# Kernel tuning notes

Measured on AMD Instinct MI355X. Metric: run time of the kernel, lower is better.

The kernel has to match this reference:

```python
import jax, jax.numpy as jnp
import numpy as np

MIN_SPARSITY = 0.05
MAX_SPARSITY = 0.3


def setup_inputs() -> dict:
    key = jax.random.key(0)
    k1, k2, k3 = jax.random.split(key, 3)
    B, D = 4096, 4096
    H = D // 4
    x = jax.random.normal(k1, (B, D), dtype=jnp.float32)
    W1 = jax.random.normal(k2, (D, H), dtype=jnp.float32) * (1.0 / np.sqrt(D))
    b1 = jnp.zeros((H,), dtype=jnp.float32)
    W2 = jax.random.normal(k3, (H, 1), dtype=jnp.float32) * (1.0 / np.sqrt(H))
    b2 = jnp.zeros((1,), dtype=jnp.float32)
    return {"x": x, "W1": W1, "b1": b1, "W2": W2, "b2": b2}


def reference(x, W1, b1, W2, b2):
    B, D = x.shape
    # learned per-row sparsity in [min, max]
    h = jax.nn.relu(x @ W1 + b1)                      # [B, D//4]
    s = jax.nn.sigmoid(h @ W2 + b2)                   # [B, 1]
    sparsity = MIN_SPARSITY + (MAX_SPARSITY - MIN_SPARSITY) * s  # [B, 1]

    # per-row kth smallest |x| as threshold; k = max(1, round(D*(1-sparsity)))
    abs_x = jnp.abs(x)
    sorted_abs = jnp.sort(abs_x, axis=1)              # [B, D] ascending
    k = jnp.round(D * (1.0 - sparsity[:, 0])).astype(jnp.int32)
    k = jnp.clip(k, 1, D)
    threshold = jnp.take_along_axis(sorted_abs, (k - 1)[:, None], axis=1)  # [B, 1]

    mask = (abs_x > threshold).astype(x.dtype)        # [B, D]
    sparse_x = x * mask
    actual_sparsity = mask.sum(axis=1) / D            # [B]
    l1_reg = jnp.abs(sparse_x).sum(axis=1).mean()     # scalar
    return sparse_x, mask, sparsity, actual_sparsity, l1_reg
```

## Files before the change

### kernel.cpp

```cpp
#include <hip/hip_runtime.h>
#include <hip/hip_fp8.h>

typedef __attribute__((ext_vector_type(4))) float f32x4;


__device__ __forceinline__ unsigned char f2fp8(float f) {
    return (unsigned char)__hip_cvt_float_to_fp8(f, __HIP_SATFINITE, __HIP_E4M3);
}

__device__ __forceinline__ void gl16(const void* g, void* l) {
    __builtin_amdgcn_global_load_lds(
        (const __attribute__((address_space(1))) void*)g,
        (__attribute__((address_space(3))) void*)l, 16, 0, 0);
}

__global__ __launch_bounds__(256) void k0a_cvtx(const float* __restrict__ x,
                                                unsigned char* __restrict__ xa_t)
{
    const int bm = blockIdx.x;
    const int ktbase = blockIdx.y * 16;
    const int t = threadIdx.x;
    const int rr = t >> 2, q = t & 3;
    const int kgp = q ^ ((rr >> 1) & 3);
    const size_t rowoff = (size_t)(bm * 64 + rr) * 4096;

    #pragma unroll
    for (int i = 0; i < 16; i++) {
        const int kt = ktbase + i;
        const float* src = x + rowoff + kt * 32 + q * 8;
        float4 v0 = *(const float4*)src;
        float4 v1 = *(const float4*)(src + 4);
        union { unsigned char c[8]; uint2 u; } o;
        o.c[0] = f2fp8(v0.x); o.c[1] = f2fp8(v0.y);
        o.c[2] = f2fp8(v0.z); o.c[3] = f2fp8(v0.w);
        o.c[4] = f2fp8(v1.x); o.c[5] = f2fp8(v1.y);
        o.c[6] = f2fp8(v1.z); o.c[7] = f2fp8(v1.w);
        *(uint2*)(xa_t + ((size_t)(bm * 128 + kt) * 64 + rr) * 32 + kgp * 8) = o.u;
    }
}

__global__ __launch_bounds__(256) void k0b_cvtw(const float* __restrict__ W1,
                                                unsigned char* __restrict__ wb_t)
{
    __shared__ float ls[32][128];
    const int bx = blockIdx.x;
    const int bn = bx >> 7, kt = bx & 127;
    const int t = threadIdx.x;

    #pragma unroll
    for (int i = 0; i < 4; i++) {
        int s = t + i * 256;
        int r = s >> 5, c4 = s & 31;
        *(float4*)&ls[r][c4 * 4] =
            *(const float4*)(W1 + (size_t)(kt * 32 + r) * 1024 + bn * 128 + c4 * 4);
    }
    __syncthreads();

    const int n = t >> 1, half = t & 1;
    #pragma unroll
    for (int kg2 = 0; kg2 < 2; kg2++) {
        const int kg = half * 2 + kg2;
        const int kgp = kg ^ ((n >> 1) & 3);
        union { unsigned char c[8]; uint2 u; } o;
        #pragma unroll
        for (int j = 0; j < 8; j++) o.c[j] = f2fp8(ls[kg * 8 + j][n] * 64.0f);
        *(uint2*)(wb_t + (size_t)(bn * 128 + kt) * 4096 + n * 32 + kgp * 8) = o.u;
    }
}

__global__ __launch_bounds__(512, 4) void k1est(const unsigned char* __restrict__ xa_t,
                                                const unsigned char* __restrict__ wb_t,
                                                const float* __restrict__ b1,
                                                const float* __restrict__ W2,
                                                float* __restrict__ plogit)
{
    __shared__ alignas(16) unsigned char Ab[4][4096];
    __shared__ alignas(16) unsigned char Bb[4][8192];

    const int bid = blockIdx.x;
    const int wgid = (bid & 7) * 64 + (bid >> 3);
    const int bn = wgid >> 6, bm = wgid & 63;
    const int tid = threadIdx.x;
    const int l = tid & 63, w = tid >> 6;
    const int wm = w & 3, wn = w >> 2;
    const int arow = l & 15, kg = l >> 4;
    const int kgs = kg ^ ((arow >> 1) & 3);
    const bool stager = (w < 4);

    const unsigned char* abase = xa_t + (size_t)bm * 128 * 2048;
    const unsigned char* bbase = wb_t + (size_t)bn * 128 * 4096;

    f32x4 acc[4];
    #pragma unroll
    for (int j = 0; j < 4; j++) acc[j] = (f32x4)0.0f;

#define ISSUE(step, buf)                                                          \
    if (stager) {                                                                 \
        gl16(abase + (size_t)(step) * 4096 + tid * 16, &Ab[buf][tid * 16]);       \
        gl16(bbase + (size_t)(step) * 8192 + tid * 16, &Bb[buf][tid * 16]);       \
        gl16(bbase + (size_t)(step) * 8192 + (256 + tid) * 16,                    \
             &Bb[buf][(256 + tid) * 16]);                                         \
    }

    ISSUE(0, 0);
    ISSUE(1, 1);

    for (int t = 0; t < 64; t++) {
        const int buf = t & 3;
        if (t <= 61) {
            ISSUE(t + 2, (t + 2) & 3);
            asm volatile("s_waitcnt vmcnt(6)" ::: "memory");
        } else if (t == 62) {
            asm volatile("s_waitcnt vmcnt(3)" ::: "memory");
        } else {
            asm volatile("s_waitcnt vmcnt(0)" ::: "memory");
        }
        __builtin_amdgcn_s_barrier();
        __builtin_amdgcn_sched_barrier(0);

        #pragma unroll
        for (int j = 0; j < 2; j++) {
            long af = *(const long*)&Ab[buf][j * 2048 + (wm * 16 + arow) * 32 + kgs * 8];
            #pragma unroll
            for (int nf = 0; nf < 4; nf++) {
                long bf = *(const long*)&Bb[buf][j * 4096 +
                                                 (wn * 64 + nf * 16 + arow) * 32 + kgs * 8];
                acc[nf] = __builtin_amdgcn_mfma_f32_16x16x32_fp8_fp8(af, bf, acc[nf], 0, 0, 0);
            }
        }
    }
#undef ISSUE

    float p[4] = {0.0f, 0.0f, 0.0f, 0.0f};
    #pragma unroll
    for (int nf = 0; nf < 4; nf++) {
        const int n = bn * 128 + wn * 64 + nf * 16 + arow;
        const float bb = b1[n], ww = W2[n];
        #pragma unroll
        for (int i = 0; i < 4; i++) {
            float h = acc[nf][i] * 0.015625f + bb;
            if (h > 0.0f) p[i] += h * ww;
        }
    }
    #pragma unroll
    for (int i = 0; i < 4; i++) {
        #pragma unroll
        for (int o = 1; o < 16; o <<= 1) p[i] += __shfl_xor(p[i], o, 64);
        if (arow == 0) {
            const int row = bm * 64 + wm * 16 + kg * 4 + i;
            plogit[(size_t)row * 16 + bn * 2 + wn] = p[i];
        }
    }
}

__global__ __launch_bounds__(256) void k2_row(const float* __restrict__ x,
                                              const float* __restrict__ plogit,
                                              const float* __restrict__ b2,
                                              float* __restrict__ out_sparse,
                                              float* __restrict__ out_mask,
                                              float* __restrict__ out_spars,
                                              float* __restrict__ out_actual,
                                              double* __restrict__ l1rows)
{
    __shared__ unsigned hist[2048];
    __shared__ unsigned cand[512];
    __shared__ unsigned wsum[4];
    __shared__ int cnt_w[4];
    __shared__ double l1_w[4];
    __shared__ unsigned sel_s, selexc_s;
    __shared__ int k_s;

    const int row = blockIdx.x;
    const int tid = threadIdx.x;
    const int lane = tid & 63, wid = tid >> 6;
    const float* xr = x + (size_t)row * 4096;

    for (int i = tid; i < 2048; i += 256) hist[i] = 0;
    if (tid == 0) {
        float lg = 0.0f;
        #pragma unroll
        for (int t = 0; t < 16; t++) lg += plogit[(size_t)row * 16 + t];
        double s  = 1.0 / (1.0 + exp(-(double)(lg + b2[0])));
        double sp = 0.05 + 0.25 * s;
        int k = (int)rint(4096.0 * (1.0 - sp));
        if (k < 1) k = 1;
        if (k > 4096) k = 4096;
        k_s = k;
        out_spars[row] = (float)sp;
    }
    __syncthreads();

    uint4 rv[4];
    #pragma unroll
    for (int j = 0; j < 4; j++) {
        rv[j] = ((const uint4*)xr)[tid + j * 256];
        atomicAdd(&hist[(rv[j].x & 0x7fffffffu) >> 20], 1u);
        atomicAdd(&hist[(rv[j].y & 0x7fffffffu) >> 20], 1u);
        atomicAdd(&hist[(rv[j].z & 0x7fffffffu) >> 20], 1u);
        atomicAdd(&hist[(rv[j].w & 0x7fffffffu) >> 20], 1u);
    }
    __syncthreads();

    int krem = k_s;
    unsigned prefix = 0;
    {
        const unsigned base = tid * 8;
        unsigned bl[8];
        unsigned v = 0;
        #pragma unroll
        for (int j = 0; j < 8; j++) { bl[j] = hist[base + j]; v += bl[j]; }
        unsigned sc = v;
        #pragma unroll
        for (int o = 1; o < 64; o <<= 1) {
            unsigned n = __shfl_up(sc, o, 64);
            if (lane >= o) sc += n;
        }
        if (lane == 63) wsum[wid] = sc;
        __syncthreads();
        unsigned off = 0;
        for (int ww = 0; ww < wid; ww++) off += wsum[ww];
        sc += off;
        unsigned exc = sc - v;
        if ((int)sc >= krem && (int)exc < krem) {
            unsigned run = exc;
            #pragma unroll
            for (int j = 0; j < 8; j++) {
                if ((int)run < krem && (int)(run + bl[j]) >= krem) {
                    sel_s = base + j; selexc_s = run;
                }
                run += bl[j];
            }
        }
        __syncthreads();
        prefix = sel_s;
        krem -= (int)selexc_s;
        __syncthreads();
    }

    int cntm = 0;
    #pragma unroll
    for (int j = 0; j < 4; j++)
        #pragma unroll
        for (int e = 0; e < 4; e++) {
            unsigned a = (&rv[j].x)[e] & 0x7fffffffu;
            if ((a >> 20) == prefix) cntm++;
        }
    unsigned sc2 = (unsigned)cntm;
    #pragma unroll
    for (int o = 1; o < 64; o <<= 1) {
        unsigned n = __shfl_up(sc2, o, 64);
        if (lane >= o) sc2 += n;
    }
    if (lane == 63) wsum[wid] = sc2;
    __syncthreads();
    unsigned off2 = 0;
    for (int ww = 0; ww < wid; ww++) off2 += wsum[ww];
    unsigned pos = sc2 + off2 - (unsigned)cntm;
    const int nc = (int)(wsum[0] + wsum[1] + wsum[2] + wsum[3]);
    #pragma unroll
    for (int j = 0; j < 4; j++)
        #pragma unroll
        for (int e = 0; e < 4; e++) {
            unsigned a = (&rv[j].x)[e] & 0x7fffffffu;
            if ((a >> 20) == prefix) { if (pos < 512) cand[pos] = a; pos++; }
        }
    __syncthreads();
    const bool usec = (nc <= 512);

    #pragma unroll
    for (int p = 0; p < 3; p++) {
        const int shift = (p == 0) ? 12 : (p == 1) ? 4 : 0;
        const int width = (p == 2) ? 4 : 8;
        const int nb = 1 << width;
        const int topshift = shift + width;
        if (tid < nb) hist[tid] = 0;
        __syncthreads();
        if (usec) {
            for (int i = tid; i < nc; i += 256) {
                unsigned a = cand[i];
                if ((a >> topshift) == prefix)
                    atomicAdd(&hist[(a >> shift) & (nb - 1)], 1u);
            }
        } else {
            #pragma unroll
            for (int j = 0; j < 4; j++) {
                #pragma unroll
                for (int e = 0; e < 4; e++) {
                    unsigned a = (&rv[j].x)[e] & 0x7fffffffu;
                    if ((a >> topshift) == prefix)
                        atomicAdd(&hist[(a >> shift) & (nb - 1)], 1u);
                }
            }
        }
        __syncthreads();
        unsigned v = (tid < nb) ? hist[tid] : 0;
        unsigned sc = v;
        #pragma unroll
        for (int o = 1; o < 64; o <<= 1) {
            unsigned n = __shfl_up(sc, o, 64);
            if (lane >= o) sc += n;
        }
        if (lane == 63) wsum[wid] = sc;
        __syncthreads();
        unsigned off = 0;
        for (int ww = 0; ww < wid; ww++) off += wsum[ww];
        sc += off;
        unsigned exc = sc - v;
        if ((int)sc >= krem && (int)exc < krem) { sel_s = (unsigned)tid; selexc_s = exc; }
        __syncthreads();
        prefix = (prefix << width) | sel_s;
        krem -= (int)selexc_s;
        __syncthreads();
    }
    const unsigned thr = prefix;

    int cnt = 0;
    double l1 = 0.0;
    float* os = out_sparse + (size_t)row * 4096;
    float* om = out_mask + (size_t)row * 4096;
    #pragma unroll
    for (int j = 0; j < 4; j++) {
        float4 sv, mv;
        #pragma unroll
        for (int e = 0; e < 4; e++) {
            unsigned b = (&rv[j].x)[e];
            unsigned a = b & 0x7fffffffu;
            bool m = a > thr;
            (&sv.x)[e] = m ? __uint_as_float(b) : 0.0f;
            (&mv.x)[e] = m ? 1.0f : 0.0f;
            if (m) { cnt++; l1 += (double)__uint_as_float(a); }
        }
        ((float4*)os)[tid + j * 256] = sv;
        ((float4*)om)[tid + j * 256] = mv;
    }
    #pragma unroll
    for (int o = 32; o > 0; o >>= 1) {
        cnt += __shfl_down(cnt, o, 64);
        l1  += __shfl_down(l1,  o, 64);
    }
    if (lane == 0) { cnt_w[wid] = cnt; l1_w[wid] = l1; }
    __syncthreads();
    if (tid == 0) {
        int c    = cnt_w[0] + cnt_w[1] + cnt_w[2] + cnt_w[3];
        double l = l1_w[0] + l1_w[1] + l1_w[2] + l1_w[3];
        out_actual[row] = (float)c / 4096.0f;
        l1rows[row] = l;
    }
}

__global__ __launch_bounds__(1024) void k3_l1(const double* __restrict__ l1rows,
                                              float* __restrict__ out_l1)
{
    __shared__ double sm[1024];
    int tid = threadIdx.x;
    double s = l1rows[tid] + l1rows[tid + 1024] + l1rows[tid + 2048] + l1rows[tid + 3072];
    sm[tid] = s;
    __syncthreads();
    for (int st = 512; st > 0; st >>= 1) {
        if (tid < st) sm[tid] += sm[tid + st];
        __syncthreads();
    }
    if (tid == 0) out_l1[0] = (float)(sm[0] / 4096.0);
}

extern "C" void kernel_launch(void* const* d_in, const int* in_sizes, int n_in,
                              void* d_out, int out_size, void* d_ws, size_t ws_size,
                              hipStream_t stream)
{
    const float* x  = (const float*)d_in[0];
    const float* W1 = (const float*)d_in[1];
    const float* b1 = (const float*)d_in[2];
    const float* W2 = (const float*)d_in[3];
    const float* b2 = (const float*)d_in[4];

    float* out        = (float*)d_out;
    float* out_sparse = out;
    float* out_mask   = out + 16777216;
    float* out_spars  = out + 33554432;
    float* out_actual = out + 33558528;
    float* out_l1     = out + 33562624;

    unsigned char* xa_t = (unsigned char*)(out);
    unsigned char* wb_t = (unsigned char*)(out + 4194304);

    char* ws = (char*)d_ws;
    float*  plogit = (float*)(ws);
    double* l1rows = (double*)(ws + 262144);

    k0a_cvtx<<<dim3(64, 8), 256, 0, stream>>>(x, xa_t);
    k0b_cvtw<<<1024, 256, 0, stream>>>(W1, wb_t);
    k1est<<<512, 512, 0, stream>>>(xa_t, wb_t, b1, W2, plogit);
    k2_row<<<4096, 256, 0, stream>>>(x, plogit, b2, out_sparse, out_mask,
                                     out_spars, out_actual, l1rows);
    k3_l1<<<1, 1024, 0, stream>>>(l1rows, out_l1);
}
```

Baseline: 109.7 us.

## Split row selection and mask application into separate kernels with nontemporal stores

Splits the per-row threshold-selection kernel into two: one finds the per-row threshold and stores it to workspace, and a second re-reads x and writes the sparse and mask outputs with nontemporal stores. The aim is to shorten the selection kernel and let the write-heavy phase run at full occupancy with streaming stores. In exchange, x is read from global memory a second time and there is an extra kernel launch.

```diff
diff --git a/kernel.cpp b/kernel.cpp
--- a/kernel.cpp
+++ b/kernel.cpp
@@ -2,6 +2,7 @@
 #include <hip/hip_fp8.h>
 
 typedef __attribute__((ext_vector_type(4))) float f32x4;
+typedef __attribute__((ext_vector_type(4))) unsigned u32x4;
 
 
 __device__ __forceinline__ unsigned char f2fp8(float f) {
@@ -153,20 +154,15 @@
     }
 }
 
-__global__ __launch_bounds__(256) void k2_row(const float* __restrict__ x,
-                                              const float* __restrict__ plogit,
-                                              const float* __restrict__ b2,
-                                              float* __restrict__ out_sparse,
-                                              float* __restrict__ out_mask,
-                                              float* __restrict__ out_spars,
-                                              float* __restrict__ out_actual,
-                                              double* __restrict__ l1rows)
+__global__ __launch_bounds__(256) void k2a_sel(const float* __restrict__ x,
+                                               const float* __restrict__ plogit,
+                                               const float* __restrict__ b2,
+                                               unsigned* __restrict__ thr_arr,
+                                               float* __restrict__ out_spars)
 {
     __shared__ unsigned hist[2048];
     __shared__ unsigned cand[512];
     __shared__ unsigned wsum[4];
-    __shared__ int cnt_w[4];
-    __shared__ double l1_w[4];
     __shared__ unsigned sel_s, selexc_s;
     __shared__ int k_s;
 
@@ -312,26 +308,45 @@
         krem -= (int)selexc_s;
         __syncthreads();
     }
-    const unsigned thr = prefix;
+
+    if (tid == 0) thr_arr[row] = prefix;
+}
+
+__global__ __launch_bounds__(256) void k2b_apply(const float* __restrict__ x,
+                                                 const unsigned* __restrict__ thr_arr,
+                                                 float* __restrict__ out_sparse,
+                                                 float* __restrict__ out_mask,
+                                                 float* __restrict__ out_actual,
+                                                 double* __restrict__ l1rows)
+{
+    __shared__ int cnt_w[4];
+    __shared__ double l1_w[4];
+
+    const int row = blockIdx.x;
+    const int tid = threadIdx.x;
+    const int lane = tid & 63, wid = tid >> 6;
+    const unsigned thr = thr_arr[row];
+    const float* xr = x + (size_t)row * 4096;
+    f32x4* os = (f32x4*)(out_sparse + (size_t)row * 4096);
+    f32x4* om = (f32x4*)(out_mask + (size_t)row * 4096);
 
     int cnt = 0;
     double l1 = 0.0;
-    float* os = out_sparse + (size_t)row * 4096;
-    float* om = out_mask + (size_t)row * 4096;
     #pragma unroll
     for (int j = 0; j < 4; j++) {
-        float4 sv, mv;
+        u32x4 bv = ((const u32x4*)xr)[tid + j * 256];
+        f32x4 sv, mv;
         #pragma unroll
         for (int e = 0; e < 4; e++) {
-            unsigned b = (&rv[j].x)[e];
+            unsigned b = bv[e];
             unsigned a = b & 0x7fffffffu;
             bool m = a > thr;
-            (&sv.x)[e] = m ? __uint_as_float(b) : 0.0f;
-            (&mv.x)[e] = m ? 1.0f : 0.0f;
+            sv[e] = m ? __uint_as_float(b) : 0.0f;
+            mv[e] = m ? 1.0f : 0.0f;
             if (m) { cnt++; l1 += (double)__uint_as_float(a); }
         }
-        ((float4*)os)[tid + j * 256] = sv;
-        ((float4*)om)[tid + j * 256] = mv;
+        __builtin_nontemporal_store(sv, &os[tid + j * 256]);
+        __builtin_nontemporal_store(mv, &om[tid + j * 256]);
     }
     #pragma unroll
     for (int o = 32; o > 0; o >>= 1) {
@@ -384,13 +399,15 @@
     unsigned char* wb_t = (unsigned char*)(out + 4194304);
 
     char* ws = (char*)d_ws;
-    float*  plogit = (float*)(ws);
-    double* l1rows = (double*)(ws + 262144);
+    float*    plogit  = (float*)(ws);
+    unsigned* thr_arr = (unsigned*)(ws + 262144);
+    double*   l1rows  = (double*)(ws + 278528);
 
     k0a_cvtx<<<dim3(64, 8), 256, 0, stream>>>(x, xa_t);
     k0b_cvtw<<<1024, 256, 0, stream>>>(W1, wb_t);
     k1est<<<512, 512, 0, stream>>>(xa_t, wb_t, b1, W2, plogit);
-    k2_row<<<4096, 256, 0, stream>>>(x, plogit, b2, out_sparse, out_mask,
-                                     out_spars, out_actual, l1rows);
+    k2a_sel<<<4096, 256, 0, stream>>>(x, plogit, b2, thr_arr, out_spars);
+    k2b_apply<<<4096, 256, 0, stream>>>(x, thr_arr, out_sparse, out_mask,
+                                        out_actual, l1rows);
     k3_l1<<<1, 1024, 0, stream>>>(l1rows, out_l1);
 }
```

After: 121.1 us. +10.4%, slower.
